# Performance work log

Measured on AMD Instinct MI355X. Metric: run time of the kernel, lower is better.

## Reference

```python
import jax, jax.numpy as jnp
import numpy as np

N, IN, OUT, R, E = 20000, 768, 768, 8, 320000


def setup_inputs() -> dict:
    key = jax.random.key(0)
    ks = jax.random.split(key, 9)
    x = jax.random.normal(ks[0], (N, IN), dtype=jnp.float32)
    edge_index = jax.random.randint(ks[1], (2, E), 0, N, dtype=jnp.int64)
    edge_type = jax.random.randint(ks[2], (E,), 0, R, dtype=jnp.int64)
    s1 = 1.0 / np.sqrt(IN)
    s2 = 1.0 / np.sqrt(OUT)
    W1 = jax.random.normal(ks[3], (R, IN, OUT), dtype=jnp.float32) * s1
    root1 = jax.random.normal(ks[4], (IN, OUT), dtype=jnp.float32) * s1
    b1 = jnp.zeros((OUT,), dtype=jnp.float32)
    W2 = jax.random.normal(ks[5], (R, OUT, OUT), dtype=jnp.float32) * s2
    root2 = jax.random.normal(ks[6], (OUT, OUT), dtype=jnp.float32) * s2
    b2 = jnp.zeros((OUT,), dtype=jnp.float32)
    return {"x": x, "edge_index": edge_index, "edge_type": edge_type,
            "W1": W1, "root1": root1, "b1": b1,
            "W2": W2, "root2": root2, "b2": b2}


def _rgcn_conv(x, src, dst, etype, W, root, b):
    # PyG RGCNConv: per-relation mean aggregation of neighbor features,
    # then relation-specific linear transform, plus root weight and bias.
    # mean(x_j @ W_r) == mean(x_j) @ W_r, so aggregate first, transform after.
    num_nodes = x.shape[0]
    num_rel = W.shape[0]
    x_src = x[src]                                  # [E, d_in]
    seg = dst * num_rel + etype                     # composite (node, relation) id
    sums = jax.ops.segment_sum(x_src, seg, num_segments=num_nodes * num_rel)
    cnt = jax.ops.segment_sum(jnp.ones((src.shape[0],), dtype=x.dtype), seg,
                              num_segments=num_nodes * num_rel)
    mean = sums / jnp.maximum(cnt, 1.0)[:, None]    # [N*R, d_in]
    mean = mean.reshape(num_nodes, num_rel, -1)     # [N, R, d_in]
    out = jnp.einsum('nri,rio->no', mean, W)        # relation-batched matmul
    return out + x @ root + b


def reference(x, edge_index, edge_type, W1, root1, b1, W2, root2, b2):
    src, dst = edge_index[0], edge_index[1]
    h = _rgcn_conv(x, src, dst, edge_type, W1, root1, b1)
    h = jax.nn.relu(h)
    out = _rgcn_conv(h, src, dst, edge_type, W2, root2, b2)
    return out
```

## Files before the change

kernel.cpp:

```cpp
#include <hip/hip_runtime.h>
#include <hip/hip_bf16.h>
#include <stdint.h>

#define N_NODES 20000
#define DIM     768
#define NREL    8
#define NEDGE   320000
#define NSEG    (N_NODES * NREL)
#define NSLAB   9
#define KDIM    768
#define NKT     12
#define NPW     2

typedef short short8 __attribute__((ext_vector_type(8)));
typedef float f32x4  __attribute__((ext_vector_type(4)));

__device__ __forceinline__ void async_load16(const void* g, void* l) {
  __builtin_amdgcn_global_load_lds((const __attribute__((address_space(1))) void*)g,
                                   (__attribute__((address_space(3))) void*)l,
                                   16, 0, 0);
}

__host__ __device__ __forceinline__ int imin(int a, int b) { return a < b ? a : b; }

__device__ __forceinline__ float bf_lo(uint32_t v) {
  return __builtin_bit_cast(float, v << 16);
}
__device__ __forceinline__ float bf_hi(uint32_t v) {
  return __builtin_bit_cast(float, v & 0xffff0000u);
}
__device__ __forceinline__ uint32_t pack_bf16x2(float a, float b) {
  uint32_t lo = __builtin_bit_cast(unsigned short, __float2bfloat16(a));
  uint32_t hi = __builtin_bit_cast(unsigned short, __float2bfloat16(b));
  return lo | (hi << 16);
}

__global__ void seg_count_kernel(const int* __restrict__ dst, const int* __restrict__ et,
                                 int* __restrict__ segcnt, int e_cnt) {
  int e = blockIdx.x * 256 + threadIdx.x;
  if (e < e_cnt) atomicAdd(&segcnt[dst[e] * NREL + et[e]], 1);
}

__global__ void block_scan_kernel(const int* __restrict__ in, int* __restrict__ out,
                                  int* __restrict__ partials, int n) {
  __shared__ int wsum[16];
  const int t = threadIdx.x, lane = t & 63, wave = t >> 6;
  const int i = blockIdx.x * 1024 + t;
  int v = (i < n) ? in[i] : 0;
  int s = v;
#pragma unroll
  for (int off = 1; off < 64; off <<= 1) {
    int u = __shfl_up(s, off, 64);
    if (lane >= off) s += u;
  }
  if (lane == 63) wsum[wave] = s;
  __syncthreads();
  if (t < 16) {
    int w = wsum[t];
#pragma unroll
    for (int off = 1; off < 16; off <<= 1) {
      int u = __shfl_up(w, off, 64);
      if (t >= off) w += u;
    }
    wsum[t] = w;
  }
  __syncthreads();
  const int basew = (wave > 0) ? wsum[wave - 1] : 0;
  if (i < n) out[i] = basew + s - v;
  if (t == 1023) partials[blockIdx.x] = wsum[15];
}

__global__ void partial_scan_kernel(int* __restrict__ partials, int nb) {
  const int lane = threadIdx.x & 63;
  int carry = 0;
  for (int base = 0; base < nb; base += 64) {
    const int i = base + lane;
    int v = (i < nb) ? partials[i] : 0;
    int s = v;
#pragma unroll
    for (int off = 1; off < 64; off <<= 1) {
      int u = __shfl_up(s, off, 64);
      if (lane >= off) s += u;
    }
    if (i < nb) partials[i] = carry + s - v;
    carry += __shfl(s, 63, 64);
  }
}

__global__ void add_offsets_kernel(int* __restrict__ soffs, const int* __restrict__ partials,
                                   int* __restrict__ cursor, int n) {
  const int i = blockIdx.x * 1024 + threadIdx.x;
  if (i < n) {
    const int v = soffs[i] + partials[blockIdx.x];
    soffs[i] = v;
    cursor[i] = v;
  }
  if (i == 0) soffs[n] = NEDGE;
}

__global__ void seg_scatter_kernel(const int* __restrict__ src, const int* __restrict__ dst,
                                   const int* __restrict__ et, int* __restrict__ cursor,
                                   int* __restrict__ es, int e_cnt) {
  int e = blockIdx.x * 256 + threadIdx.x;
  if (e < e_cnt) {
    const int seg = dst[e] * NREL + et[e];
    const int p = atomicAdd(&cursor[seg], 1);
    es[p] = src[e];
  }
}

__global__ void cvt_bf16_kernel(const float4* __restrict__ in, ushort4* __restrict__ out, int n4) {
  int i = blockIdx.x * 256 + threadIdx.x;
  if (i < n4) {
    float4 f = in[i];
    ushort4 r;
    r.x = __builtin_bit_cast(unsigned short, __float2bfloat16(f.x));
    r.y = __builtin_bit_cast(unsigned short, __float2bfloat16(f.y));
    r.z = __builtin_bit_cast(unsigned short, __float2bfloat16(f.z));
    r.w = __builtin_bit_cast(unsigned short, __float2bfloat16(f.w));
    out[i] = r;
  }
}

__global__ void transpose_w2_kernel(const float* __restrict__ W, const float* __restrict__ root,
                                    __hip_bfloat16* __restrict__ dst) {
  __shared__ float tile[32][33];
  const int s = blockIdx.z;
  const float* src = (s < 8) ? (W + (size_t)s * DIM * DIM) : root;
  const int c0 = blockIdx.x * 32;
  const int r0 = blockIdx.y * 32;
  const int tx = threadIdx.x, ty = threadIdx.y;
  for (int i = ty; i < 32; i += 8)
    tile[i][tx] = src[(size_t)(r0 + i) * DIM + c0 + tx];
  __syncthreads();
  for (int i = ty; i < 32; i += 8) {
    const int o = c0 + i, ii = r0 + tx;
    dst[((size_t)s * DIM + o) * KDIM + ii] = __float2bfloat16(tile[tx][i]);
  }
}

__global__ __launch_bounds__(512, 2) void gemm_kernel(
    const __hip_bfloat16* __restrict__ A,
    const __hip_bfloat16* __restrict__ BT,
    __hip_bfloat16* __restrict__ Z,
    int mvalid, int zcols) {
  __shared__ __hip_bfloat16 lds[2][2][2][128][64];

  const int t = threadIdx.x;
  const int lane = t & 63;
  const int wid = t >> 6;
  const int wave_m = wid >> 2;
  const int wave_n = wid & 3;
  const int ml = lane & 15;
  const int quad = lane >> 4;
  const int sw8 = ml & 7;
  const int lsub = lane >> 3;
  const int lg = (lane & 7) ^ lsub;
  const int wrow = wid * 8;

  const int nbx = gridDim.x;
  const int nwg = nbx * gridDim.y;
  const int lid = blockIdx.y * nbx + blockIdx.x;
  const int q = nwg >> 3, r = nwg & 7;
  const int xcd = lid & 7, off = lid >> 3;
  const int swz = (xcd < r ? xcd * (q + 1) : r * (q + 1) + (xcd - r) * q) + off;
  const int m0 = (swz / nbx) * 256;
  const int n0 = (swz % nbx) * 256;

  const char* cA = (const char*)A;
  const char* cB = (const char*)BT;
  uint32_t offA[2][2], offB[2][2];
#pragma unroll
  for (int h = 0; h < 2; ++h)
#pragma unroll
    for (int i = 0; i < 2; ++i) {
      const int srow = h * 128 + i * 64 + wrow + lsub;
      const int ar = imin(m0 + srow, mvalid - 1);
      offA[h][i] = (uint32_t)ar * (uint32_t)(KDIM * 2) + (uint32_t)(lg * 16);
      offB[h][i] = (uint32_t)(n0 + srow) * (uint32_t)(KDIM * 2) + (uint32_t)(lg * 16);
    }

#define VMCNT(N) asm volatile("s_waitcnt vmcnt(" #N ")" ::: "memory")
#define LGKM0()  asm volatile("s_waitcnt lgkmcnt(0)" ::: "memory")
#define BAR()    asm volatile("s_barrier" ::: "memory")

#define STG_A(SB, H, TS) do {                                                      \
    const char* _p = cA + (size_t)(TS) * 128;                                      \
    async_load16(_p + offA[H][0], &lds[SB][0][H][wrow][0]);                        \
    async_load16(_p + offA[H][1], &lds[SB][0][H][64 + wrow][0]);                   \
  } while (0)

#define STG_B(SB, H, TS) do {                                                      \
    const char* _p = cB + (size_t)(TS) * 128;                                      \
    async_load16(_p + offB[H][0], &lds[SB][1][H][wrow][0]);                        \
    async_load16(_p + offB[H][1], &lds[SB][1][H][64 + wrow][0]);                   \
  } while (0)

#define LOAD_A(BUF, MH, DST)                                                       \
  _Pragma("unroll") for (int mi = 0; mi < 4; ++mi)                                 \
  _Pragma("unroll") for (int kk = 0; kk < 2; ++kk)                                 \
    DST[mi][kk] = *(const short8*)&lds[BUF][0][MH][wave_m * 64 + mi * 16 + ml]     \
                                                 [((kk * 4 + quad) ^ sw8) * 8];

#define LOAD_B(BUF, NH, DST)                                                       \
  _Pragma("unroll") for (int ni = 0; ni < 2; ++ni)                                 \
  _Pragma("unroll") for (int kk = 0; kk < 2; ++kk)                                 \
    DST[ni][kk] = *(const short8*)&lds[BUF][1][NH][wave_n * 32 + ni * 16 + ml]     \
                                                 [((kk * 4 + quad) ^ sw8) * 8];

#define DO_MFMA(MH, NH, AF, BF)                                                    \
  _Pragma("unroll") for (int mi = 0; mi < 4; ++mi)                                 \
  _Pragma("unroll") for (int ni = 0; ni < 2; ++ni) {                               \
    acc[MH][NH][mi][ni] = __builtin_amdgcn_mfma_f32_16x16x32_bf16(                 \
        AF[mi][0], BF[ni][0], acc[MH][NH][mi][ni], 0, 0, 0);                       \
    acc[MH][NH][mi][ni] = __builtin_amdgcn_mfma_f32_16x16x32_bf16(                 \
        AF[mi][1], BF[ni][1], acc[MH][NH][mi][ni], 0, 0, 0);                       \
  }

  f32x4 acc[2][2][4][2] = {};
  short8 aA[4][2], aB[4][2];
  short8 b0[2][2], b1[2][2];

  STG_A(0, 0, 0); STG_B(0, 0, 0);
  STG_B(0, 1, 0);
  STG_A(0, 1, 0);
  STG_A(1, 0, 1); STG_B(1, 0, 1);
  STG_B(1, 1, 1);
  STG_A(1, 1, 1);
  VMCNT(12);
  BAR();
  LOAD_A(0, 0, aA);
  LOAD_B(0, 0, b0);
  VMCNT(8);
  BAR();

  for (int T = 0; T < NKT; ++T) {
    const int buf = T & 1;
    const int ts2 = (T + 2 < NKT) ? T + 2 : NKT - 1;
    VMCNT(8);
    LOAD_B(buf, 1, b1);
    BAR();
    __builtin_amdgcn_s_setprio(1);
    DO_MFMA(0, 0, aA, b0);
    __builtin_amdgcn_s_setprio(0);
    BAR();
    VMCNT(4);
    STG_A(buf, 0, ts2);
    STG_B(buf, 0, ts2);
    LOAD_A(buf, 1, aB);
    BAR();
    __builtin_amdgcn_s_setprio(1);
    DO_MFMA(0, 1, aA, b1);
    __builtin_amdgcn_s_setprio(0);
    BAR();
    STG_B(buf, 1, ts2);
    LOAD_A(buf ^ 1, 0, aA);
    BAR();
    __builtin_amdgcn_s_setprio(1);
    DO_MFMA(1, 0, aB, b0);
    __builtin_amdgcn_s_setprio(0);
    BAR();
    VMCNT(8);
    STG_A(buf, 1, ts2);
    LOAD_B(buf ^ 1, 0, b0);
    BAR();
    __builtin_amdgcn_s_setprio(1);
    DO_MFMA(1, 1, aB, b1);
    __builtin_amdgcn_s_setprio(0);
    BAR();
  }
  VMCNT(0);
  LGKM0();
  BAR();

  {
    __hip_bfloat16* sC = &lds[0][0][0][0][0];
#pragma unroll
    for (int mh = 0; mh < 2; ++mh)
#pragma unroll
      for (int mi = 0; mi < 4; ++mi)
#pragma unroll
        for (int rr = 0; rr < 4; ++rr) {
          const int row = mh * 128 + wave_m * 64 + mi * 16 + quad * 4 + rr;
          const int gx = ((row >> 2) & 3) << 4;
#pragma unroll
          for (int nh = 0; nh < 2; ++nh)
#pragma unroll
            for (int ni = 0; ni < 2; ++ni) {
              const int col = nh * 128 + wave_n * 32 + ni * 16 + ml;
              sC[row * 256 + (col ^ gx)] = __float2bfloat16(acc[mh][nh][mi][ni][rr]);
            }
        }
    BAR();
    const int rbase = wid * 32 + (lane >> 5);
    const int col = (lane & 31) * 8;
#pragma unroll
    for (int it = 0; it < 16; ++it) {
      const int row = rbase + it * 2;
      const int scol = ((((col >> 4) ^ ((row >> 2) & 3)) << 4) | (col & 15));
      short8 v = *(const short8*)&sC[row * 256 + scol];
      const int grow = m0 + row;
      if (grow < mvalid)
        *(short8*)(Z + (size_t)grow * (size_t)zcols + (size_t)(n0 + col)) = v;
    }
  }

#undef VMCNT
#undef LGKM0
#undef BAR
#undef STG_A
#undef STG_B
#undef LOAD_A
#undef LOAD_B
#undef DO_MFMA
}

__device__ __forceinline__ void seg_mean_add(const char* cZ, size_t zrb, uint32_t colb,
                                             int beg, int end, int boff, float* acc,
                                             const int* es) {
  float s[12];
#pragma unroll
  for (int i = 0; i < 12; ++i) s[i] = 0.f;
  int e = beg;
  for (; e + 2 <= end; e += 2) {
    const int s0 = es[e], s1 = es[e + 1];
    const char* p0 = cZ + (size_t)s0 * zrb + colb + boff;
    const char* p1 = cZ + (size_t)s1 * zrb + colb + boff;
    const uint2 a0 = *(const uint2*)(p0);
    const uint2 a1 = *(const uint2*)(p0 + 512);
    const uint2 a2 = *(const uint2*)(p0 + 1024);
    const uint2 c0 = *(const uint2*)(p1);
    const uint2 c1 = *(const uint2*)(p1 + 512);
    const uint2 c2 = *(const uint2*)(p1 + 1024);
    s[0]  += bf_lo(a0.x); s[1]  += bf_hi(a0.x);
    s[2]  += bf_lo(a0.y); s[3]  += bf_hi(a0.y);
    s[4]  += bf_lo(a1.x); s[5]  += bf_hi(a1.x);
    s[6]  += bf_lo(a1.y); s[7]  += bf_hi(a1.y);
    s[8]  += bf_lo(a2.x); s[9]  += bf_hi(a2.x);
    s[10] += bf_lo(a2.y); s[11] += bf_hi(a2.y);
    s[0]  += bf_lo(c0.x); s[1]  += bf_hi(c0.x);
    s[2]  += bf_lo(c0.y); s[3]  += bf_hi(c0.y);
    s[4]  += bf_lo(c1.x); s[5]  += bf_hi(c1.x);
    s[6]  += bf_lo(c1.y); s[7]  += bf_hi(c1.y);
    s[8]  += bf_lo(c2.x); s[9]  += bf_hi(c2.x);
    s[10] += bf_lo(c2.y); s[11] += bf_hi(c2.y);
  }
  if (e < end) {
    const int s0 = es[e];
    const char* p0 = cZ + (size_t)s0 * zrb + colb + boff;
    const uint2 a0 = *(const uint2*)(p0);
    const uint2 a1 = *(const uint2*)(p0 + 512);
    const uint2 a2 = *(const uint2*)(p0 + 1024);
    s[0]  += bf_lo(a0.x); s[1]  += bf_hi(a0.x);
    s[2]  += bf_lo(a0.y); s[3]  += bf_hi(a0.y);
    s[4]  += bf_lo(a1.x); s[5]  += bf_hi(a1.x);
    s[6]  += bf_lo(a1.y); s[7]  += bf_hi(a1.y);
    s[8]  += bf_lo(a2.x); s[9]  += bf_hi(a2.x);
    s[10] += bf_lo(a2.y); s[11] += bf_hi(a2.y);
  }
  const float inv = 1.f / (float)(end - beg);
#pragma unroll
  for (int i = 0; i < 12; ++i) acc[i] += s[i] * inv;
}

__global__ __launch_bounds__(256) void aggregate2_kernel(
    const __hip_bfloat16* __restrict__ Z,
    int zcols,
    const int* __restrict__ soffs, const int* __restrict__ es,
    const float* __restrict__ bias,
    float* __restrict__ accf,
    __hip_bfloat16* __restrict__ outb,
    int g0, int ns, int first, int last, int mode) {
  const int t = threadIdx.x;
  const int lane = t & 63;
  const int wave = t >> 6;
  const int boff = lane * 8;
  const char* cZ = (const char*)Z;
  const size_t zrb = (size_t)zcols * 2;

  int n = (blockIdx.x * 4 + wave) * NPW;
  for (int it = 0; it < NPW; ++it, ++n) {
    if (n >= N_NODES) return;
    float acc[12];
    if (first) {
      const float4 bv0 = *(const float4*)(bias + lane * 4);
      const float4 bv1 = *(const float4*)(bias + 256 + lane * 4);
      const float4 bv2 = *(const float4*)(bias + 512 + lane * 4);
      acc[0] = bv0.x; acc[1] = bv0.y; acc[2] = bv0.z; acc[3] = bv0.w;
      acc[4] = bv1.x; acc[5] = bv1.y; acc[6] = bv1.z; acc[7] = bv1.w;
      acc[8] = bv2.x; acc[9] = bv2.y; acc[10] = bv2.z; acc[11] = bv2.w;
    } else {
      const float* ap = accf + (size_t)n * DIM;
      const float4 v0 = *(const float4*)(ap + lane * 4);
      const float4 v1 = *(const float4*)(ap + 256 + lane * 4);
      const float4 v2 = *(const float4*)(ap + 512 + lane * 4);
      acc[0] = v0.x; acc[1] = v0.y; acc[2] = v0.z; acc[3] = v0.w;
      acc[4] = v1.x; acc[5] = v1.y; acc[6] = v1.z; acc[7] = v1.w;
      acc[8] = v2.x; acc[9] = v2.y; acc[10] = v2.z; acc[11] = v2.w;
    }
    const int rend = imin(g0 + ns, NREL);
    for (int r = g0; r < rend; ++r) {
      const int beg = soffs[n * NREL + r], end = soffs[n * NREL + r + 1];
      if (beg == end) continue;
      seg_mean_add(cZ, zrb, (uint32_t)(r - g0) * (DIM * 2), beg, end, boff, acc, es);
    }
    if (last) {
      const char* zr = cZ + (size_t)n * zrb + (size_t)(NSLAB - 1 - g0) * (DIM * 2);
      const uint2 r0 = *(const uint2*)(zr + boff);
      const uint2 r1 = *(const uint2*)(zr + boff + 512);
      const uint2 r2 = *(const uint2*)(zr + boff + 1024);
      acc[0] += bf_lo(r0.x); acc[1] += bf_hi(r0.x);
      acc[2] += bf_lo(r0.y); acc[3] += bf_hi(r0.y);
      acc[4] += bf_lo(r1.x); acc[5] += bf_hi(r1.x);
      acc[6] += bf_lo(r1.y); acc[7] += bf_hi(r1.y);
      acc[8] += bf_lo(r2.x); acc[9] += bf_hi(r2.x);
      acc[10] += bf_lo(r2.y); acc[11] += bf_hi(r2.y);
    }
    if (!last) {
      float* ap = accf + (size_t)n * DIM;
      float4 v0, v1, v2;
      v0.x = acc[0]; v0.y = acc[1]; v0.z = acc[2]; v0.w = acc[3];
      v1.x = acc[4]; v1.y = acc[5]; v1.z = acc[6]; v1.w = acc[7];
      v2.x = acc[8]; v2.y = acc[9]; v2.z = acc[10]; v2.w = acc[11];
      *(float4*)(ap + lane * 4) = v0;
      *(float4*)(ap + 256 + lane * 4) = v1;
      *(float4*)(ap + 512 + lane * 4) = v2;
    } else if (mode == 0) {
      char* dst = (char*)outb + (size_t)n * (DIM * 2);
      uint2 o0, o1, o2;
      o0.x = pack_bf16x2(fmaxf(acc[0], 0.f), fmaxf(acc[1], 0.f));
      o0.y = pack_bf16x2(fmaxf(acc[2], 0.f), fmaxf(acc[3], 0.f));
      o1.x = pack_bf16x2(fmaxf(acc[4], 0.f), fmaxf(acc[5], 0.f));
      o1.y = pack_bf16x2(fmaxf(acc[6], 0.f), fmaxf(acc[7], 0.f));
      o2.x = pack_bf16x2(fmaxf(acc[8], 0.f), fmaxf(acc[9], 0.f));
      o2.y = pack_bf16x2(fmaxf(acc[10], 0.f), fmaxf(acc[11], 0.f));
      *(uint2*)(dst + boff) = o0;
      *(uint2*)(dst + boff + 512) = o1;
      *(uint2*)(dst + boff + 1024) = o2;
    } else {
      float* ap = accf + (size_t)n * DIM;
      float4 v0, v1, v2;
      v0.x = acc[0]; v0.y = acc[1]; v0.z = acc[2]; v0.w = acc[3];
      v1.x = acc[4]; v1.y = acc[5]; v1.z = acc[6]; v1.w = acc[7];
      v2.x = acc[8]; v2.y = acc[9]; v2.z = acc[10]; v2.w = acc[11];
      *(float4*)(ap + lane * 4) = v0;
      *(float4*)(ap + 256 + lane * 4) = v1;
      *(float4*)(ap + 512 + lane * 4) = v2;
    }
  }
}

extern "C" void kernel_launch(void* const* d_in, const int* in_sizes, int n_in,
                              void* d_out, int out_size, void* d_ws, size_t ws_size,
                              hipStream_t stream) {
  const float* x     = (const float*)d_in[0];
  const int*   eidx  = (const int*)d_in[1];
  const int*   etype = (const int*)d_in[2];
  const float* W1    = (const float*)d_in[3];
  const float* root1 = (const float*)d_in[4];
  const float* b1    = (const float*)d_in[5];
  const float* W2    = (const float*)d_in[6];
  const float* root2 = (const float*)d_in[7];
  const float* b2    = (const float*)d_in[8];
  float* out = (float*)d_out;
  const int* esrc_in = eidx;
  const int* edst_in = eidx + NEDGE;

  char* p = (char*)d_ws;
  auto alloc = [&](size_t bytes) -> char* {
    char* r = p;
    p += (bytes + 255) & ~(size_t)255;
    return r;
  };
  __hip_bfloat16* wt  = (__hip_bfloat16*)alloc((size_t)NSLAB * DIM * KDIM * 2);
  int* segcnt   = (int*)alloc((size_t)NSEG * 4);
  int* soffs    = (int*)alloc((size_t)(NSEG + 1) * 4);
  int* cursor   = (int*)alloc((size_t)NSEG * 4);
  int* partials = (int*)alloc(256 * 4);
  int* es       = (int*)alloc((size_t)NEDGE * 4);
  __hip_bfloat16* xb  = (__hip_bfloat16*)alloc((size_t)N_NODES * DIM * 2);
  __hip_bfloat16* hb  = xb;

  const size_t used = (size_t)(p - (char*)d_ws);
  const size_t remain = (ws_size > used) ? (ws_size - used) : 0;
  const size_t slab_bytes = (size_t)N_NODES * DIM * 2;
  int S = (int)(remain / slab_bytes);
  if (S > NSLAB) S = NSLAB;
  if (S < 1) S = 1;
  __hip_bfloat16* Z = (__hip_bfloat16*)p;

  const int NB = (NSEG + 1023) / 1024;
  (void)hipMemsetAsync(segcnt, 0, (size_t)NSEG * 4, stream);
  seg_count_kernel<<<(NEDGE + 255) / 256, 256, 0, stream>>>(edst_in, etype, segcnt, NEDGE);
  block_scan_kernel<<<NB, 1024, 0, stream>>>(segcnt, soffs, partials, NSEG);
  partial_scan_kernel<<<1, 64, 0, stream>>>(partials, NB);
  add_offsets_kernel<<<NB, 1024, 0, stream>>>(soffs, partials, cursor, NSEG);
  seg_scatter_kernel<<<(NEDGE + 255) / 256, 256, 0, stream>>>(esrc_in, edst_in, etype, cursor, es, NEDGE);

  cvt_bf16_kernel<<<((N_NODES * DIM / 4) + 255) / 256, 256, 0, stream>>>(
      (const float4*)x, (ushort4*)xb, N_NODES * DIM / 4);
  dim3 tb(32, 8);
  transpose_w2_kernel<<<dim3(DIM / 32, DIM / 32, NSLAB), tb, 0, stream>>>(W1, root1, wt);

  const int agrid = (N_NODES + 4 * NPW - 1) / (4 * NPW);

  for (int g0 = 0; g0 < NSLAB; g0 += S) {
    const int ns = imin(S, NSLAB - g0);
    const int zc = ns * DIM;
    dim3 gg(zc / 256, (N_NODES + 255) / 256);
    gemm_kernel<<<gg, 512, 0, stream>>>(xb, wt + (size_t)g0 * DIM * KDIM, Z, N_NODES, zc);
    aggregate2_kernel<<<agrid, 256, 0, stream>>>(Z, zc, soffs, es, b1, out, hb,
                                                 g0, ns, g0 == 0, g0 + ns == NSLAB, 0);
  }

  transpose_w2_kernel<<<dim3(DIM / 32, DIM / 32, NSLAB), tb, 0, stream>>>(W2, root2, wt);

  for (int g0 = 0; g0 < NSLAB; g0 += S) {
    const int ns = imin(S, NSLAB - g0);
    const int zc = ns * DIM;
    dim3 gg(zc / 256, (N_NODES + 255) / 256);
    gemm_kernel<<<gg, 512, 0, stream>>>(hb, wt + (size_t)g0 * DIM * KDIM, Z, N_NODES, zc);
    aggregate2_kernel<<<agrid, 256, 0, stream>>>(Z, zc, soffs, es, b2, out, nullptr,
                                                 g0, ns, g0 == 0, g0 + ns == NSLAB, 1);
  }
}
```

Baseline: 914.5 us.

## Restructure GEMM main loop into two-tile unrolled four-phase schedule with nontemporal stores

The bf16 MFMA GEMM main loop is unrolled by two K-tiles and split into four phases. Each phase loads both A and B fragments from LDS, issues global-to-LDS staging for a future tile, and then runs two MFMA blocks under raised priority. This halves the number of barriers per MFMA block, and a third B register set is added so the fragments persist across phases. Output stores now use nontemporal hints so the result does not pollute the cache; the cost is more live registers and a changed overlap of LDS reads with staging writes.

```diff
diff --git a/kernel.cpp b/kernel.cpp
--- a/kernel.cpp
+++ b/kernel.cpp
@@ -219,52 +219,58 @@
 
   f32x4 acc[2][2][4][2] = {};
   short8 aA[4][2], aB[4][2];
-  short8 b0[2][2], b1[2][2];
+  short8 b0a[2][2], b0b[2][2], b1[2][2];
 
   STG_A(0, 0, 0); STG_B(0, 0, 0);
-  STG_B(0, 1, 0);
-  STG_A(0, 1, 0);
+  STG_A(0, 1, 0); STG_B(0, 1, 0);
   STG_A(1, 0, 1); STG_B(1, 0, 1);
-  STG_B(1, 1, 1);
-  STG_A(1, 1, 1);
+  STG_A(1, 1, 1); STG_B(1, 1, 1);
   VMCNT(12);
   BAR();
   LOAD_A(0, 0, aA);
-  LOAD_B(0, 0, b0);
-  VMCNT(8);
+  LOAD_B(0, 0, b0a);
   BAR();
 
-  for (int T = 0; T < NKT; ++T) {
-    const int buf = T & 1;
+  for (int T = 0; T < NKT; T += 2) {
     const int ts2 = (T + 2 < NKT) ? T + 2 : NKT - 1;
+    const int ts3 = (T + 3 < NKT) ? T + 3 : NKT - 1;
     VMCNT(8);
-    LOAD_B(buf, 1, b1);
+    LOAD_A(0, 1, aB);
+    LOAD_B(0, 1, b1);
+    STG_A(0, 0, ts2); STG_B(0, 0, ts2);
     BAR();
     __builtin_amdgcn_s_setprio(1);
-    DO_MFMA(0, 0, aA, b0);
-    __builtin_amdgcn_s_setprio(0);
-    BAR();
-    VMCNT(4);
-    STG_A(buf, 0, ts2);
-    STG_B(buf, 0, ts2);
-    LOAD_A(buf, 1, aB);
-    BAR();
-    __builtin_amdgcn_s_setprio(1);
+    DO_MFMA(0, 0, aA, b0a);
     DO_MFMA(0, 1, aA, b1);
     __builtin_amdgcn_s_setprio(0);
     BAR();
-    STG_B(buf, 1, ts2);
-    LOAD_A(buf ^ 1, 0, aA);
+    VMCNT(8);
+    LOAD_A(1, 0, aA);
+    LOAD_B(1, 0, b0b);
+    STG_A(0, 1, ts2); STG_B(0, 1, ts2);
     BAR();
     __builtin_amdgcn_s_setprio(1);
-    DO_MFMA(1, 0, aB, b0);
+    DO_MFMA(1, 0, aB, b0a);
+    DO_MFMA(1, 1, aB, b1);
     __builtin_amdgcn_s_setprio(0);
     BAR();
     VMCNT(8);
-    STG_A(buf, 1, ts2);
-    LOAD_B(buf ^ 1, 0, b0);
+    LOAD_A(1, 1, aB);
+    LOAD_B(1, 1, b1);
+    STG_A(1, 0, ts3); STG_B(1, 0, ts3);
     BAR();
     __builtin_amdgcn_s_setprio(1);
+    DO_MFMA(0, 0, aA, b0b);
+    DO_MFMA(0, 1, aA, b1);
+    __builtin_amdgcn_s_setprio(0);
+    BAR();
+    VMCNT(8);
+    LOAD_A(0, 0, aA);
+    LOAD_B(0, 0, b0a);
+    STG_A(1, 1, ts3); STG_B(1, 1, ts3);
+    BAR();
+    __builtin_amdgcn_s_setprio(1);
+    DO_MFMA(1, 0, aB, b0b);
     DO_MFMA(1, 1, aB, b1);
     __builtin_amdgcn_s_setprio(0);
     BAR();
@@ -301,7 +307,8 @@
       short8 v = *(const short8*)&sC[row * 256 + scol];
       const int grow = m0 + row;
       if (grow < mvalid)
-        *(short8*)(Z + (size_t)grow * (size_t)zcols + (size_t)(n0 + col)) = v;
+        __builtin_nontemporal_store(
+            v, (short8*)(Z + (size_t)grow * (size_t)zcols + (size_t)(n0 + col)));
     }
   }
 
```

Result: slower. 1.564 ms (+71.1%).
